# Performance work log

Measured on AMD Instinct MI355X. Metric: run time of the kernel, lower is better.

The kernel has to match this reference:

```python
import jax, jax.numpy as jnp
import numpy as np

# hyperparams matching init_kwargs
T_LEN = 1024
T_LATENCY = 7
TB = T_LATENCY + 1          # t_len_block
N_OUT = 1024
BATCH = 32
FS_SCALE = 10.0             # FastSigmoid default scale


@jax.custom_vjp
def fast_sigmoid(x):
    # forward: Heaviside; backward: fast-sigmoid surrogate
    return (x > 0).astype(x.dtype)

def _fs_fwd(x):
    return (x > 0).astype(x.dtype), x

def _fs_bwd(x, g):
    return (g / (FS_SCALE * jnp.abs(x) + 1.0) ** 2,)

fast_sigmoid.defvjp(_fs_fwd, _fs_bwd)


def setup_inputs() -> dict:
    key = jax.random.key(0)
    k1, k2, k3, k4 = jax.random.split(key, 4)
    x = jax.random.normal(k1, (T_LEN, BATCH, N_OUT), dtype=jnp.float32) * 0.6
    # raw params; forward applies the clamp/abs 'properties' of the module
    beta_raw = jax.random.uniform(k2, (N_OUT,), minval=0.7, maxval=0.99, dtype=jnp.float32)
    p_raw = jax.random.uniform(k3, (N_OUT,), minval=0.5, maxval=0.95, dtype=jnp.float32)
    b_raw = jax.random.uniform(k4, (N_OUT,), minval=0.2, maxval=1.0, dtype=jnp.float32)
    return {"x": x, "beta_raw": beta_raw, "p_raw": p_raw, "b_raw": b_raw}


def reference(x, beta_raw, p_raw, b_raw):
    T, B, N = x.shape
    tb = TB
    n_blocks = T // tb  # t_pad == 0 by construction
    dt = x.dtype

    # clamped properties
    beta = jnp.clip(beta_raw, 0.001, 0.999)          # [N]
    p = jnp.clip(jnp.abs(p_raw), 0.0, 0.999)         # [N]
    bb = jnp.clip(jnp.abs(b_raw), 0.001, 1.0)        # [N]

    t_idx = jnp.arange(tb)
    expo = t_idx[:, None] - t_idx[None, :]            # [tb,tb], t - s
    lower = expo >= 0
    # causal decay kernel: beta^(t-s) for s<=t  (grouped conv1d equivalent)
    beta_pow = jnp.where(lower[:, :, None],
                         beta[None, None, :] ** jnp.maximum(expo, 0)[:, :, None].astype(dt),
                         jnp.zeros((), dt))           # [tb,tb,N]
    # phi kernel: weight (t-s+1) for s<=t  (conv2d equivalent)
    phi = jnp.where(lower, (expo + 1).astype(dt), jnp.zeros((), dt))  # [tb,tb]
    p_exp = jnp.arange(1, tb + 1, dtype=dt)           # [tb]
    p_pow = p[None, :] ** p_exp[:, None]              # [tb,N]
    inv_p = 1.0 / p                                   # [N]

    def body(carry, x_slice):
        spikes, z, int_mem, a_kernel = carry          # [tb,B,N],[tb,B,N],[B,N],[tb,B,N]
        sg = jax.lax.stop_gradient(spikes)            # detach_spike_grad=True
        maskf = (jnp.max(sg, axis=0) > 0).astype(dt)  # [B,N] any spike in prev block
        # refractory masking of input
        xs = jnp.where(z < maskf[None], jnp.zeros((), dt), x_slice)
        v_init = int_mem * (1.0 - maskf)
        # adaptation update
        a_at_spike = jnp.sum(a_kernel * sg, axis=0) + inv_p          # [B,N]
        decay_steps = jnp.sum(z > 1, axis=0).astype(dt)              # [B,N]
        new_a = a_at_spike * jnp.power(p[None, :], decay_steps)
        a = a_kernel[-1] * (1.0 - maskf) + new_a * maskf             # [B,N]
        a_k = p_pow[:, None, :] * a[None]                             # [tb,B,N]
        v_th = 1.0 + bb[None, None, :] * a_k                          # [tb,B,N]
        # --- Block forward ---
        cur = xs.at[0].add(beta[None, :] * v_init)
        membrane = jnp.einsum('tsn,sbn->tbn', beta_pow, cur)          # causal decayed sum
        faulty = fast_sigmoid(membrane - v_th)                        # [tb,B,N] 0/1
        z_new = jnp.einsum('ts,sbn->tbn', phi, faulty)
        # g(): keep only entries exactly 1, straight-through grad
        spikes_new = z_new - jax.lax.stop_gradient(
            jnp.where(z_new == 1.0, jnp.zeros((), dt), z_new))
        return (spikes_new, z_new, membrane[-1], a_k), spikes_new

    z0 = jnp.zeros((tb, B, N), dt)
    carry0 = (z0, z0, jnp.zeros((B, N), dt), z0)
    xb = x.reshape(n_blocks, tb, B, N)
    _, out = jax.lax.scan(body, carry0, xb)
    return out.reshape(T, B, N)
```

## Files before the change

### kernel.cpp

```cpp
#include <hip/hip_runtime.h>


constexpr int T_LEN = 1024;
constexpr int TB    = 8;
constexpr int NBLK  = T_LEN / TB;
constexpr int BATCH = 32;
constexpr int NOUT  = 1024;
constexpr int BN    = BATCH * NOUT;
constexpr int G     = 4;
constexpr int NITER = NBLK / G;
constexpr int RING  = 16;

typedef float f4 __attribute__((ext_vector_type(4)));

__device__ __forceinline__ void dma16(const float* g, float* l) {
    __builtin_amdgcn_global_load_lds(
        (const __attribute__((address_space(1))) void*)g,
        (__attribute__((address_space(3))) void*)l, 16, 0, 0);
}

__global__ __launch_bounds__(128, 1)
void snn_blocks_kernel(const float* __restrict__ x,
                       const float* __restrict__ beta_raw,
                       const float* __restrict__ p_raw,
                       const float* __restrict__ b_raw,
                       float* __restrict__ out)
{
    __shared__ float inbuf[RING][TB * 64];
    __shared__ float sbuf[2][G][TB * 64];

    const int tid  = threadIdx.x;
    const int lane = tid & 63;
    const int wid  = tid >> 6;
    const int wg0  = blockIdx.x * 64;

    if (wid == 1) {
        const int rowoff = lane >> 4;
        const int coloff = wg0 + (lane & 15) * 4;
        const float* xbase = x   + (ptrdiff_t)rowoff * BN + coloff;
        float*       obase = out + (ptrdiff_t)rowoff * BN + coloff;

        auto dmaGroup = [&](int j2) {
#pragma unroll
            for (int i = 0; i < G; ++i) {
                const int b = j2 * G + i;
                const float* g = xbase + (ptrdiff_t)(b * TB) * BN;
                float* l = &inbuf[b & (RING - 1)][0];
                dma16(g,          l);
                dma16(g + 4 * BN, l + 256);
            }
        };
        auto drainIter = [&](int j) {
#pragma unroll
            for (int i = 0; i < G; ++i) {
                const float* sf = &sbuf[j & 1][i][0];
                f4 s0 = *(const f4*)(sf + lane * 4);
                f4 s1 = *(const f4*)(sf + 256 + lane * 4);
                const int b = j * G + i;
                *(f4*)(obase + (ptrdiff_t)(b * TB) * BN)     = s0;
                *(f4*)(obase + (ptrdiff_t)(b * TB + 4) * BN) = s1;
            }
        };

        dmaGroup(0);
        dmaGroup(1);
        asm volatile("s_waitcnt vmcnt(8)" ::: "memory");
        __builtin_amdgcn_s_barrier();
        asm volatile("" ::: "memory");

        dmaGroup(2);
        asm volatile("s_waitcnt vmcnt(8)" ::: "memory");
        __builtin_amdgcn_s_barrier();
        asm volatile("" ::: "memory");

#pragma unroll 1
        for (int j = 1; j <= 29; ++j) {
            drainIter(j - 1);
            dmaGroup(j + 2);
            asm volatile("s_waitcnt vmcnt(16)" ::: "memory");
            __builtin_amdgcn_s_barrier();
            asm volatile("" ::: "memory");
        }

        drainIter(29);
        asm volatile("s_waitcnt vmcnt(8)" ::: "memory");
        __builtin_amdgcn_s_barrier();
        asm volatile("" ::: "memory");

        drainIter(30);
        __builtin_amdgcn_s_barrier();
        asm volatile("" ::: "memory");

        drainIter(31);
    } else {
        const int gid = wg0 + lane;
        const int n   = gid & (NOUT - 1);

        double beta = (double)beta_raw[n];
        beta = beta < 0.001 ? 0.001 : (beta > 0.999 ? 0.999 : beta);
        double p = fabs((double)p_raw[n]);
        p = p > 0.999 ? 0.999 : p;
        double bb = fabs((double)b_raw[n]);
        bb = bb < 0.001 ? 0.001 : (bb > 1.0 ? 1.0 : bb);
        const double inv_p = 1.0 / p;

        double ppow[9];
        ppow[0] = 1.0;
#pragma unroll
        for (int i = 1; i <= 8; ++i) ppow[i] = ppow[i - 1] * p;
        double bbp[8];
#pragma unroll
        for (int t = 0; t < 8; ++t) bbp[t] = bb * ppow[t + 1];
        const double pp2 = ppow[2], pp4 = ppow[4], pp8 = ppow[8];

        double m = 0.0, a = 0.0;
        int maskf = 0, firstp = 0;

        __builtin_amdgcn_s_barrier();
        asm volatile("" ::: "memory");

#pragma unroll 1
        for (int j = 0; j < NITER; ++j) {
            const int g0 = (j & 3) * G;

#pragma unroll
            for (int i = 0; i < G; ++i) {
                float cur[8];
#pragma unroll
                for (int t = 0; t < 8; ++t)
                    cur[t] = inbuf[g0 + i][t * 64 + lane];

                double pf1 = p;
                pf1 *= (firstp & 1) ? p   : 1.0;
                pf1 *= (firstp & 2) ? pp2 : 1.0;
                pf1 *= (firstp & 4) ? pp4 : 1.0;
                const int dsteps = firstp ^ 7;
                double pd = (dsteps & 1) ? p : 1.0;
                pd *= (dsteps & 2) ? pp2 : 1.0;
                pd *= (dsteps & 4) ? pp4 : 1.0;
                const double new_a = (a * pf1 + inv_p) * pd;
                double vinit;
                if (maskf) { a = new_a;   vinit = 0.0; }
                else       { a = pp8 * a; vinit = m;   }

                const int zmask = maskf ? ((1 << firstp) - 1) : 0;

                int fbits = 0;
                double mm = vinit;
#pragma unroll
                for (int t = 0; t < 8; ++t) {
                    const float xf = ((zmask >> t) & 1) ? 0.0f : cur[t];
                    mm = beta * mm + (double)xf;
                    const double vth = 1.0 + bbp[t] * a;
                    fbits |= (mm - vth > 0.0) ? (1 << t) : 0;
                }
                m = mm;
                maskf  = (fbits != 0);
                firstp = fbits ? __builtin_ctz(fbits) : 0;

#pragma unroll
                for (int t = 0; t < 8; ++t)
                    sbuf[j & 1][i][t * 64 + lane] =
                        (maskf && t == firstp) ? 1.0f : 0.0f;
            }

            asm volatile("s_waitcnt lgkmcnt(0)" ::: "memory");
            __builtin_amdgcn_s_barrier();
            asm volatile("" ::: "memory");
        }
    }
}

extern "C" void kernel_launch(void* const* d_in, const int* in_sizes, int n_in,
                              void* d_out, int out_size, void* d_ws, size_t ws_size,
                              hipStream_t stream) {
    const float* x        = (const float*)d_in[0];
    const float* beta_raw = (const float*)d_in[1];
    const float* p_raw    = (const float*)d_in[2];
    const float* b_raw    = (const float*)d_in[3];
    float* out            = (float*)d_out;

    dim3 grid(BN / 64);
    dim3 block(128);
    snn_blocks_kernel<<<grid, block, 0, stream>>>(x, beta_raw, p_raw, b_raw, out);
}
```

Measured before the change: 237.3 us.

## Process two independent neuron columns per compute lane with 128-column tiles

Each workgroup now covers 128 columns instead of 64, and each compute lane runs two independent neuron recurrences interleaved. This gives the serial double-precision dependency chain instruction-level parallelism to hide latency, and the DMA and store rows widen to 512 bytes. The grid halves to 256 workgroups, which roughly matches the CU count but lowers occupancy and doubles LDS use per workgroup.

```diff
diff --git a/kernel.cpp b/kernel.cpp
--- a/kernel.cpp
+++ b/kernel.cpp
@@ -10,6 +10,8 @@
 constexpr int G     = 4;
 constexpr int NITER = NBLK / G;
 constexpr int RING  = 16;
+constexpr int CPW   = 128;
+constexpr int TILE  = TB * CPW;
 
 typedef float f4 __attribute__((ext_vector_type(4)));
 
@@ -26,50 +28,55 @@
                        const float* __restrict__ b_raw,
                        float* __restrict__ out)
 {
-    __shared__ float inbuf[RING][TB * 64];
-    __shared__ float sbuf[2][G][TB * 64];
+    __shared__ float inbuf[RING][TILE];
+    __shared__ float sbuf[2][G][TILE];
 
     const int tid  = threadIdx.x;
     const int lane = tid & 63;
     const int wid  = tid >> 6;
-    const int wg0  = blockIdx.x * 64;
+    const int wg0  = blockIdx.x * CPW;
 
     if (wid == 1) {
-        const int rowoff = lane >> 4;
-        const int coloff = wg0 + (lane & 15) * 4;
-        const float* xbase = x   + (ptrdiff_t)rowoff * BN + coloff;
-        float*       obase = out + (ptrdiff_t)rowoff * BN + coloff;
+        const int rowsel = lane >> 5;
+        const int col4   = (lane & 31) * 4;
+        const float* xb = x   + wg0 + col4;
+        float*       ob = out + wg0 + col4;
 
         auto dmaGroup = [&](int j2) {
 #pragma unroll
             for (int i = 0; i < G; ++i) {
                 const int b = j2 * G + i;
-                const float* g = xbase + (ptrdiff_t)(b * TB) * BN;
-                float* l = &inbuf[b & (RING - 1)][0];
-                dma16(g,          l);
-                dma16(g + 4 * BN, l + 256);
+                float* tile = &inbuf[b & (RING - 1)][0];
+#pragma unroll
+                for (int s = 0; s < 4; ++s) {
+                    const float* g =
+                        xb + (ptrdiff_t)(b * TB + 2 * s + rowsel) * BN;
+                    dma16(g, tile + s * 256);
+                }
             }
         };
         auto drainIter = [&](int j) {
 #pragma unroll
             for (int i = 0; i < G; ++i) {
+                const int b = j * G + i;
                 const float* sf = &sbuf[j & 1][i][0];
-                f4 s0 = *(const f4*)(sf + lane * 4);
-                f4 s1 = *(const f4*)(sf + 256 + lane * 4);
-                const int b = j * G + i;
-                *(f4*)(obase + (ptrdiff_t)(b * TB) * BN)     = s0;
-                *(f4*)(obase + (ptrdiff_t)(b * TB + 4) * BN) = s1;
+#pragma unroll
+                for (int s = 0; s < 4; ++s) {
+                    f4 v = *(const f4*)(sf + s * 256 + lane * 4);
+                    *(f4*)(ob + (ptrdiff_t)(b * TB + 2 * s + rowsel) * BN)
+                        = v;
+                }
             }
         };
 
         dmaGroup(0);
         dmaGroup(1);
-        asm volatile("s_waitcnt vmcnt(8)" ::: "memory");
+        asm volatile("s_waitcnt vmcnt(16)" ::: "memory");
         __builtin_amdgcn_s_barrier();
         asm volatile("" ::: "memory");
 
         dmaGroup(2);
-        asm volatile("s_waitcnt vmcnt(8)" ::: "memory");
+        asm volatile("s_waitcnt vmcnt(16)" ::: "memory");
         __builtin_amdgcn_s_barrier();
         asm volatile("" ::: "memory");
 
@@ -83,7 +90,7 @@
         }
 
         drainIter(29);
-        asm volatile("s_waitcnt vmcnt(8)" ::: "memory");
+        asm volatile("s_waitcnt vmcnt(16)" ::: "memory");
         __builtin_amdgcn_s_barrier();
         asm volatile("" ::: "memory");
 
@@ -93,28 +100,32 @@
 
         drainIter(31);
     } else {
-        const int gid = wg0 + lane;
-        const int n   = gid & (NOUT - 1);
-
-        double beta = (double)beta_raw[n];
-        beta = beta < 0.001 ? 0.001 : (beta > 0.999 ? 0.999 : beta);
-        double p = fabs((double)p_raw[n]);
-        p = p > 0.999 ? 0.999 : p;
-        double bb = fabs((double)b_raw[n]);
-        bb = bb < 0.001 ? 0.001 : (bb > 1.0 ? 1.0 : bb);
-        const double inv_p = 1.0 / p;
-
-        double ppow[9];
-        ppow[0] = 1.0;
-#pragma unroll
-        for (int i = 1; i <= 8; ++i) ppow[i] = ppow[i - 1] * p;
-        double bbp[8];
-#pragma unroll
-        for (int t = 0; t < 8; ++t) bbp[t] = bb * ppow[t + 1];
-        const double pp2 = ppow[2], pp4 = ppow[4], pp8 = ppow[8];
-
-        double m = 0.0, a = 0.0;
-        int maskf = 0, firstp = 0;
+        double pC[2], pp2C[2], pp4C[2], pp8C[2], invpC[2], betaC[2];
+        double bbpC[2][8];
+#pragma unroll
+        for (int c = 0; c < 2; ++c) {
+            const int n = (wg0 + c * 64 + lane) & (NOUT - 1);
+            double beta = (double)beta_raw[n];
+            beta = beta < 0.001 ? 0.001 : (beta > 0.999 ? 0.999 : beta);
+            double p = fabs((double)p_raw[n]);
+            p = p > 0.999 ? 0.999 : p;
+            double bb = fabs((double)b_raw[n]);
+            bb = bb < 0.001 ? 0.001 : (bb > 1.0 ? 1.0 : bb);
+            double ppow[9];
+            ppow[0] = 1.0;
+#pragma unroll
+            for (int i = 1; i <= 8; ++i) ppow[i] = ppow[i - 1] * p;
+#pragma unroll
+            for (int t = 0; t < 8; ++t) bbpC[c][t] = bb * ppow[t + 1];
+            betaC[c] = beta;   pC[c]   = p;
+            pp2C[c]  = ppow[2]; pp4C[c] = ppow[4]; pp8C[c] = ppow[8];
+            invpC[c] = 1.0 / p;
+        }
+
+        double m[2]  = {0.0, 0.0};
+        double a[2]  = {0.0, 0.0};
+        int maskf[2]  = {0, 0};
+        int firstp[2] = {0, 0};
 
         __builtin_amdgcn_s_barrier();
         asm volatile("" ::: "memory");
@@ -125,43 +136,50 @@
 
 #pragma unroll
             for (int i = 0; i < G; ++i) {
-                float cur[8];
-#pragma unroll
-                for (int t = 0; t < 8; ++t)
-                    cur[t] = inbuf[g0 + i][t * 64 + lane];
-
-                double pf1 = p;
-                pf1 *= (firstp & 1) ? p   : 1.0;
-                pf1 *= (firstp & 2) ? pp2 : 1.0;
-                pf1 *= (firstp & 4) ? pp4 : 1.0;
-                const int dsteps = firstp ^ 7;
-                double pd = (dsteps & 1) ? p : 1.0;
-                pd *= (dsteps & 2) ? pp2 : 1.0;
-                pd *= (dsteps & 4) ? pp4 : 1.0;
-                const double new_a = (a * pf1 + inv_p) * pd;
-                double vinit;
-                if (maskf) { a = new_a;   vinit = 0.0; }
-                else       { a = pp8 * a; vinit = m;   }
-
-                const int zmask = maskf ? ((1 << firstp) - 1) : 0;
-
-                int fbits = 0;
-                double mm = vinit;
-#pragma unroll
-                for (int t = 0; t < 8; ++t) {
-                    const float xf = ((zmask >> t) & 1) ? 0.0f : cur[t];
-                    mm = beta * mm + (double)xf;
-                    const double vth = 1.0 + bbp[t] * a;
-                    fbits |= (mm - vth > 0.0) ? (1 << t) : 0;
+                const float* tile = &inbuf[g0 + i][0];
+                float cur[2][8];
+#pragma unroll
+                for (int c = 0; c < 2; ++c)
+#pragma unroll
+                    for (int t = 0; t < 8; ++t)
+                        cur[c][t] = tile[t * CPW + c * 64 + lane];
+
+#pragma unroll
+                for (int c = 0; c < 2; ++c) {
+                    double pf1 = pC[c];
+                    pf1 *= (firstp[c] & 1) ? pC[c]   : 1.0;
+                    pf1 *= (firstp[c] & 2) ? pp2C[c] : 1.0;
+                    pf1 *= (firstp[c] & 4) ? pp4C[c] : 1.0;
+                    const int dsteps = firstp[c] ^ 7;
+                    double pd = (dsteps & 1) ? pC[c] : 1.0;
+                    pd *= (dsteps & 2) ? pp2C[c] : 1.0;
+                    pd *= (dsteps & 4) ? pp4C[c] : 1.0;
+                    const double new_a = (a[c] * pf1 + invpC[c]) * pd;
+                    double vinit;
+                    if (maskf[c]) { a[c] = new_a;          vinit = 0.0;  }
+                    else          { a[c] = pp8C[c] * a[c]; vinit = m[c]; }
+
+                    const int zmask = maskf[c] ? ((1 << firstp[c]) - 1) : 0;
+
+                    int fbits = 0;
+                    double mm = vinit;
+#pragma unroll
+                    for (int t = 0; t < 8; ++t) {
+                        const float xf =
+                            ((zmask >> t) & 1) ? 0.0f : cur[c][t];
+                        mm = betaC[c] * mm + (double)xf;
+                        const double vth = 1.0 + bbpC[c][t] * a[c];
+                        fbits |= (mm - vth > 0.0) ? (1 << t) : 0;
+                    }
+                    m[c] = mm;
+                    maskf[c]  = (fbits != 0);
+                    firstp[c] = fbits ? __builtin_ctz(fbits) : 0;
+
+#pragma unroll
+                    for (int t = 0; t < 8; ++t)
+                        sbuf[j & 1][i][t * CPW + c * 64 + lane] =
+                            (maskf[c] && t == firstp[c]) ? 1.0f : 0.0f;
                 }
-                m = mm;
-                maskf  = (fbits != 0);
-                firstp = fbits ? __builtin_ctz(fbits) : 0;
-
-#pragma unroll
-                for (int t = 0; t < 8; ++t)
-                    sbuf[j & 1][i][t * 64 + lane] =
-                        (maskf && t == firstp) ? 1.0f : 0.0f;
             }
 
             asm volatile("s_waitcnt lgkmcnt(0)" ::: "memory");
@@ -180,7 +198,7 @@
     const float* b_raw    = (const float*)d_in[3];
     float* out            = (float*)d_out;
 
-    dim3 grid(BN / 64);
+    dim3 grid(BN / CPW);
     dim3 block(128);
     snn_blocks_kernel<<<grid, block, 0, stream>>>(x, beta_raw, p_raw, b_raw, out);
 }
```

Measured after the change: 268.9 us. 13.3% more time.

## Write spikes directly from compute wave and double DMA group size

Applied to the files above, without the earlier changes.

The compute wave now stores spike outputs straight to global memory with per-lane scalar stores. This removes the LDS staging buffer and the producer wave's drain step. The DMA group size grows from 4 to 8 blocks and the ring from 16 to 32 tiles, which halves the number of barriers. All eight blocks of input are loaded from LDS into registers before compute, which raises register pressure, and the output stores become 4-byte lane-contiguous writes instead of 16-byte vector stores.

```diff
diff --git a/kernel.cpp b/kernel.cpp
--- a/kernel.cpp
+++ b/kernel.cpp
@@ -7,11 +7,9 @@
 constexpr int BATCH = 32;
 constexpr int NOUT  = 1024;
 constexpr int BN    = BATCH * NOUT;
-constexpr int G     = 4;
+constexpr int G     = 8;
 constexpr int NITER = NBLK / G;
-constexpr int RING  = 16;
-
-typedef float f4 __attribute__((ext_vector_type(4)));
+constexpr int RING  = 32;
 
 __device__ __forceinline__ void dma16(const float* g, float* l) {
     __builtin_amdgcn_global_load_lds(
@@ -27,7 +25,6 @@
                        float* __restrict__ out)
 {
     __shared__ float inbuf[RING][TB * 64];
-    __shared__ float sbuf[2][G][TB * 64];
 
     const int tid  = threadIdx.x;
     const int lane = tid & 63;
@@ -37,64 +34,40 @@
     if (wid == 1) {
         const int rowoff = lane >> 4;
         const int coloff = wg0 + (lane & 15) * 4;
-        const float* xbase = x   + (ptrdiff_t)rowoff * BN + coloff;
-        float*       obase = out + (ptrdiff_t)rowoff * BN + coloff;
+        const float* xbase = x + (ptrdiff_t)rowoff * BN + coloff;
 
-        auto dmaGroup = [&](int j2) {
+        auto dmaGroup = [&](int jg) {
 #pragma unroll
             for (int i = 0; i < G; ++i) {
-                const int b = j2 * G + i;
+                const int b = jg * G + i;
+                float* tile = &inbuf[(jg & 3) * G + i][0];
                 const float* g = xbase + (ptrdiff_t)(b * TB) * BN;
-                float* l = &inbuf[b & (RING - 1)][0];
-                dma16(g,          l);
-                dma16(g + 4 * BN, l + 256);
-            }
-        };
-        auto drainIter = [&](int j) {
-#pragma unroll
-            for (int i = 0; i < G; ++i) {
-                const float* sf = &sbuf[j & 1][i][0];
-                f4 s0 = *(const f4*)(sf + lane * 4);
-                f4 s1 = *(const f4*)(sf + 256 + lane * 4);
-                const int b = j * G + i;
-                *(f4*)(obase + (ptrdiff_t)(b * TB) * BN)     = s0;
-                *(f4*)(obase + (ptrdiff_t)(b * TB + 4) * BN) = s1;
+                dma16(g,          tile);
+                dma16(g + 4 * BN, tile + 256);
             }
         };
 
         dmaGroup(0);
         dmaGroup(1);
-        asm volatile("s_waitcnt vmcnt(8)" ::: "memory");
-        __builtin_amdgcn_s_barrier();
-        asm volatile("" ::: "memory");
-
-        dmaGroup(2);
-        asm volatile("s_waitcnt vmcnt(8)" ::: "memory");
+        asm volatile("s_waitcnt vmcnt(16)" ::: "memory");
         __builtin_amdgcn_s_barrier();
         asm volatile("" ::: "memory");
 
 #pragma unroll 1
-        for (int j = 1; j <= 29; ++j) {
-            drainIter(j - 1);
+        for (int j = 0; j <= 13; ++j) {
             dmaGroup(j + 2);
             asm volatile("s_waitcnt vmcnt(16)" ::: "memory");
             __builtin_amdgcn_s_barrier();
             asm volatile("" ::: "memory");
         }
-
-        drainIter(29);
-        asm volatile("s_waitcnt vmcnt(8)" ::: "memory");
+        asm volatile("s_waitcnt vmcnt(0)" ::: "memory");
         __builtin_amdgcn_s_barrier();
         asm volatile("" ::: "memory");
-
-        drainIter(30);
         __builtin_amdgcn_s_barrier();
-        asm volatile("" ::: "memory");
-
-        drainIter(31);
     } else {
         const int gid = wg0 + lane;
         const int n   = gid & (NOUT - 1);
+        float* ob = out + gid;
 
         double beta = (double)beta_raw[n];
         beta = beta < 0.001 ? 0.001 : (beta > 0.999 ? 0.999 : beta);
@@ -121,14 +94,19 @@
 
 #pragma unroll 1
         for (int j = 0; j < NITER; ++j) {
-            const int g0 = (j & 3) * G;
+            const int s0 = (j & 3) * G;
+
+            float cur[G][8];
+#pragma unroll
+            for (int i = 0; i < G; ++i)
+#pragma unroll
+                for (int t = 0; t < 8; ++t)
+                    cur[i][t] = inbuf[s0 + i][t * 64 + lane];
+            asm volatile("s_waitcnt lgkmcnt(0)" ::: "memory");
 
 #pragma unroll
             for (int i = 0; i < G; ++i) {
-                float cur[8];
-#pragma unroll
-                for (int t = 0; t < 8; ++t)
-                    cur[t] = inbuf[g0 + i][t * 64 + lane];
+                const int blk = j * G + i;
 
                 double pf1 = p;
                 pf1 *= (firstp & 1) ? p   : 1.0;
@@ -149,7 +127,7 @@
                 double mm = vinit;
 #pragma unroll
                 for (int t = 0; t < 8; ++t) {
-                    const float xf = ((zmask >> t) & 1) ? 0.0f : cur[t];
+                    const float xf = ((zmask >> t) & 1) ? 0.0f : cur[i][t];
                     mm = beta * mm + (double)xf;
                     const double vth = 1.0 + bbp[t] * a;
                     fbits |= (mm - vth > 0.0) ? (1 << t) : 0;
@@ -159,12 +137,12 @@
                 firstp = fbits ? __builtin_ctz(fbits) : 0;
 
 #pragma unroll
-                for (int t = 0; t < 8; ++t)
-                    sbuf[j & 1][i][t * 64 + lane] =
-                        (maskf && t == firstp) ? 1.0f : 0.0f;
+                for (int t = 0; t < 8; ++t) {
+                    const float sv = (maskf && t == firstp) ? 1.0f : 0.0f;
+                    ob[(ptrdiff_t)(blk * TB + t) * BN] = sv;
+                }
             }
 
-            asm volatile("s_waitcnt lgkmcnt(0)" ::: "memory");
             __builtin_amdgcn_s_barrier();
             asm volatile("" ::: "memory");
         }
```

After: 241.7 us. About the same (+1.9%).
